# Kernel optimization log

Hardware: AMD Instinct MI355X
Metric: run time of the kernel (lower is better)

The kernel has to match this reference:

```python
import jax, jax.numpy as jnp
import numpy as np

B, S, E, H = 2, 2048, 2048, 32
D = E // H  # head_dim = 64
SCALE = D ** -0.5


def setup_inputs() -> dict:
    key = jax.random.key(0)
    ks = jax.random.split(key, 9)
    std = E ** -0.5
    return {
        "hidden_states": jax.random.normal(ks[0], (B, S, E), dtype=jnp.float32),
        "Wq": jax.random.normal(ks[1], (E, E), dtype=jnp.float32) * std,
        "bq": jax.random.normal(ks[2], (E,), dtype=jnp.float32) * 0.02,
        "Wk": jax.random.normal(ks[3], (E, E), dtype=jnp.float32) * std,
        "bk": jax.random.normal(ks[4], (E,), dtype=jnp.float32) * 0.02,
        "Wv": jax.random.normal(ks[5], (E, E), dtype=jnp.float32) * std,
        "bv": jax.random.normal(ks[6], (E,), dtype=jnp.float32) * 0.02,
        "Wo": jax.random.normal(ks[7], (E, E), dtype=jnp.float32) * std,
        "bo": jax.random.normal(ks[8], (E,), dtype=jnp.float32) * 0.02,
    }


def reference(hidden_states, Wq, bq, Wk, bk, Wv, bv, Wo, bo):
    # QKV projections (torch Linear: x @ W.T + b)
    q = hidden_states @ Wq.T + bq  # [B,S,E]
    k = hidden_states @ Wk.T + bk
    v = hidden_states @ Wv.T + bv
    # split heads -> [B,S,H,D]
    q = q.reshape(B, S, H, D)
    k = k.reshape(B, S, H, D)
    v = v.reshape(B, S, H, D)
    # causal scaled dot-product attention (prefill path of paged attention)
    scores = jnp.einsum("bqhd,bkhd->bhqk", q, k) * SCALE  # [B,H,S,S]
    causal = jnp.tril(jnp.ones((S, S), dtype=bool))
    scores = jnp.where(causal, scores, jnp.finfo(scores.dtype).min)
    probs = jax.nn.softmax(scores, axis=-1)
    attn = jnp.einsum("bhqk,bkhd->bqhd", probs, v).reshape(B, S, E)
    # output projection
    return attn @ Wo.T + bo
```

## Files before the change

kernel.cpp:

```cpp
#include <hip/hip_runtime.h>
#include <hip/hip_bf16.h>

#define B_ 2
#define S_ 2048
#define E_ 2048
#define H_ 32
#define D_ 64
#define SCALE_L2E 0.18033688f

typedef __attribute__((ext_vector_type(8))) short short8_t;
typedef __attribute__((ext_vector_type(4))) float float4_t;
typedef __attribute__((ext_vector_type(16))) float f32x16;
typedef unsigned int uint;
typedef __attribute__((ext_vector_type(4))) uint uint4_t;

__device__ __forceinline__ short f2bf(float f) {
  union { float f; unsigned u; } x; x.f = f;
  unsigned r = x.u + 0x7fffu + ((x.u >> 16) & 1u);
  return (short)(r >> 16);
}

__device__ __forceinline__ void gload_lds16(const void* g, void* l) {
  __builtin_amdgcn_global_load_lds((const __attribute__((address_space(1))) void*)g,
                                   (__attribute__((address_space(3))) void*)l, 16, 0, 0);
}

__device__ __forceinline__ uint cvt_pk_bf16(float lo, float hi) {
  uint r;
  asm volatile("v_cvt_pk_bf16_f32 %0, %1, %2" : "=v"(r) : "v"(lo), "v"(hi));
  return r;
}

__device__ __forceinline__ void pl32swap(uint& a, uint& b) {
  asm volatile("v_permlane32_swap_b32 %0, %1" : "+v"(a), "+v"(b));
}

__device__ __forceinline__ f32x16 zero16() {
  f32x16 v;
#pragma unroll
  for (int i = 0; i < 16; ++i) v[i] = 0.f;
  return v;
}

__global__ void cast_xw(const float* __restrict__ X, const float* __restrict__ Wq,
                        const float* __restrict__ Wk, const float* __restrict__ Wv,
                        short* __restrict__ out) {
  constexpr int nX = 1 << 21, nW = 1 << 20, total = nX + 3 * nW;
  const int stride = gridDim.x * blockDim.x;
  for (int j = blockIdx.x * blockDim.x + threadIdx.x; j < total; j += stride) {
    const float* src;
    int idx;
    if (j < nX) {
      src = X; idx = j;
    } else {
      const int jw = j - nX;
      const int sel = jw >> 20;
      idx = jw & (nW - 1);
      src = sel == 0 ? Wq : (sel == 1 ? Wk : Wv);
    }
    const float4 v = ((const float4*)src)[idx];
    short4 r;
    r.x = f2bf(v.x); r.y = f2bf(v.y); r.z = f2bf(v.z); r.w = f2bf(v.w);
    ((short4*)out)[j] = r;
  }
}

__global__ void cast_bf16_kernel(const float* __restrict__ in, short* __restrict__ out, int n4) {
  const int stride = gridDim.x * blockDim.x;
  for (int j = blockIdx.x * blockDim.x + threadIdx.x; j < n4; j += stride) {
    const float4 v = ((const float4*)in)[j];
    short4 r;
    r.x = f2bf(v.x); r.y = f2bf(v.y); r.z = f2bf(v.z); r.w = f2bf(v.w);
    ((short4*)out)[j] = r;
  }
}

__global__ __launch_bounds__(512, 2) void gemm256_qk(const short* __restrict__ A,
                                                     const short* __restrict__ Wt,
                                                     const float* __restrict__ bq,
                                                     const float* __restrict__ bk,
                                                     short* __restrict__ Qb,
                                                     short* __restrict__ Kb) {
  extern __shared__ __align__(16) char lds[];
  constexpr int K = E_, NT = K / 64;
  const int tid = threadIdx.x, w = tid >> 6, lane = tid & 63;
  const int wr = w >> 2, wc = w & 3;
  const int m0 = blockIdx.y * 256, n0 = blockIdx.x * 256;
  const int l15 = lane & 15, l4 = lane >> 4;

  const int sr = lane >> 2;
  const int ss = lane & 3;
  const char* aB[2];
  const char* bB[2];
#pragma unroll
  for (int g = 0; g < 2; ++g) {
    const int r = w * 32 + g * 16 + sr;
    aB[g] = (const char*)A + (size_t)(m0 + r) * (K * 2) + ((ss ^ ((r >> 1) & 3)) * 16);
    bB[g] = (const char*)Wt + (size_t)(n0 + r) * (K * 2) + ((ss ^ ((r >> 1) & 3)) * 16);
  }

  auto stageA = [&](int buf, int ks, int kt) {
#pragma unroll
    for (int g = 0; g < 2; ++g)
      gload_lds16(aB[g] + kt * 128 + ks * 64, lds + (buf * 2 + ks) * 16384 + w * 2048 + g * 1024);
  };
  auto stageB = [&](int buf, int ks, int kt) {
#pragma unroll
    for (int g = 0; g < 2; ++g)
      gload_lds16(bB[g] + kt * 128 + ks * 64,
                  lds + 65536 + (buf * 2 + ks) * 16384 + w * 2048 + g * 1024);
  };
  auto ldA = [&](int buf, int ks, int i) {
    const int lr = wr * 128 + i * 16 + l15;
    return *(const short8_t*)(lds + (buf * 2 + ks) * 16384 + lr * 64 +
                              ((l4 * 16) ^ (((lr >> 1) & 3) << 4)));
  };
  auto ldB = [&](int buf, int ks, int j) {
    const int lc = wc * 64 + j * 16 + l15;
    return *(const short8_t*)(lds + 65536 + (buf * 2 + ks) * 16384 + lc * 64 +
                              ((l4 * 16) ^ (((lc >> 1) & 3) << 4)));
  };

  float4_t acc[8][4];
#pragma unroll
  for (int i = 0; i < 8; ++i)
#pragma unroll
    for (int j = 0; j < 4; ++j) acc[i][j] = (float4_t){0.f, 0.f, 0.f, 0.f};

  stageA(0, 0, 0);
  stageB(0, 0, 0);
  stageA(0, 1, 0);
  stageB(0, 1, 0);

  short8_t a_[8], b_[4];
  for (int t = 0; t < NT; ++t) {
    const int c = t & 1;
#pragma unroll
    for (int ks = 0; ks < 2; ++ks) {
      if (t + 1 < NT) {
        stageA(c ^ 1, ks, t + 1);
        stageB(c ^ 1, ks, t + 1);
        asm volatile("s_waitcnt vmcnt(8)" ::: "memory");
      } else if (ks == 0) {
        asm volatile("s_waitcnt vmcnt(4)" ::: "memory");
      } else {
        asm volatile("s_waitcnt vmcnt(0)" ::: "memory");
      }
      __builtin_amdgcn_s_barrier();
      asm volatile("" ::: "memory");
#pragma unroll
      for (int i = 0; i < 8; ++i) a_[i] = ldA(c, ks, i);
#pragma unroll
      for (int j = 0; j < 4; ++j) b_[j] = ldB(c, ks, j);
      asm volatile("s_waitcnt lgkmcnt(0)" ::: "memory");
      __builtin_amdgcn_sched_barrier(0);
      __builtin_amdgcn_s_setprio(1);
#pragma unroll
      for (int i = 0; i < 8; ++i)
#pragma unroll
        for (int j = 0; j < 4; ++j)
          acc[i][j] = __builtin_amdgcn_mfma_f32_16x16x32_bf16(a_[i], b_[j], acc[i][j], 0, 0, 0);
      __builtin_amdgcn_s_setprio(0);
    }
  }

  const int seg = n0 >> 11;
  const int ncol = n0 & 2047;
  const float* bias = seg ? bk : bq;
  short* Out = seg ? Kb : Qb;
  const float sc = seg ? 1.0f : SCALE_L2E;
  const int rg = l4 * 4;
#pragma unroll
  for (int j = 0; j < 4; ++j) {
    const int col = ncol + wc * 64 + j * 16 + l15;
    const float bvv = bias[col];
#pragma unroll
    for (int i = 0; i < 8; ++i)
#pragma unroll
      for (int ii = 0; ii < 4; ++ii)
        Out[(size_t)(m0 + wr * 128 + i * 16 + rg + ii) * E_ + col] =
            f2bf((acc[i][j][ii] + bvv) * sc);
  }
}

__global__ __launch_bounds__(512, 2) void gemm_v128(const short* __restrict__ A,
                                                    const short* __restrict__ Wt,
                                                    const float* __restrict__ bv,
                                                    short* __restrict__ Vb) {
  extern __shared__ __align__(16) char lds[];
  constexpr int K = E_, NT = K / 64;
  const int tid = threadIdx.x, w = tid >> 6, lane = tid & 63;
  const int wr = w >> 2, wc = w & 3;
  const int m0 = blockIdx.y * 128, n0 = blockIdx.x * 256;
  const int l15 = lane & 15, l4 = lane >> 4;

  const int sr = lane >> 2;
  const int ss = lane & 3;
  const char* aBase;
  const char* bBase0;
  const char* bBase1;
  {
    const int ra = w * 16 + sr;
    aBase = (const char*)A + (size_t)(m0 + ra) * (K * 2) + ((ss ^ ((ra >> 1) & 3)) * 16);
    const int rb0 = w * 16 + sr;
    bBase0 = (const char*)Wt + (size_t)(n0 + rb0) * (K * 2) + ((ss ^ ((rb0 >> 1) & 3)) * 16);
    const int rb1 = 128 + w * 16 + sr;
    bBase1 = (const char*)Wt + (size_t)(n0 + rb1) * (K * 2) + ((ss ^ ((rb1 >> 1) & 3)) * 16);
  }

  auto stageA = [&](int dbuf, int ks, int kt) {
    gload_lds16(aBase + kt * 128 + ks * 64, lds + (dbuf * 2 + ks) * 8192 + w * 1024);
  };
  auto stageB = [&](int dbuf, int ks, int kt) {
    char* base = lds + 32768 + (dbuf * 2 + ks) * 16384 + w * 1024;
    gload_lds16(bBase0 + kt * 128 + ks * 64, base);
    gload_lds16(bBase1 + kt * 128 + ks * 64, base + 8192);
  };
  auto ldA = [&](int dbuf, int ks, int i) {
    const int lr = wr * 64 + i * 16 + l15;
    return *(const short8_t*)(lds + (dbuf * 2 + ks) * 8192 + lr * 64 +
                              ((l4 * 16) ^ (((lr >> 1) & 3) << 4)));
  };
  auto ldB = [&](int dbuf, int ks, int j) {
    const int lc = wc * 64 + j * 16 + l15;
    return *(const short8_t*)(lds + 32768 + (dbuf * 2 + ks) * 16384 + lc * 64 +
                              ((l4 * 16) ^ (((lc >> 1) & 3) << 4)));
  };

  float4_t acc[4][4];
#pragma unroll
  for (int i = 0; i < 4; ++i)
#pragma unroll
    for (int j = 0; j < 4; ++j) acc[i][j] = (float4_t){0.f, 0.f, 0.f, 0.f};

  stageA(0, 0, 0);
  stageB(0, 0, 0);
  stageA(0, 1, 0);
  stageB(0, 1, 0);

  short8_t a_[4], b_[4];
  for (int t = 0; t < NT; ++t) {
    const int c = t & 1;
#pragma unroll
    for (int ks = 0; ks < 2; ++ks) {
      if (t + 1 < NT) {
        stageA(c ^ 1, ks, t + 1);
        stageB(c ^ 1, ks, t + 1);
        asm volatile("s_waitcnt vmcnt(6)" ::: "memory");
      } else if (ks == 0) {
        asm volatile("s_waitcnt vmcnt(3)" ::: "memory");
      } else {
        asm volatile("s_waitcnt vmcnt(0)" ::: "memory");
      }
      __builtin_amdgcn_s_barrier();
      asm volatile("" ::: "memory");
#pragma unroll
      for (int i = 0; i < 4; ++i) a_[i] = ldA(c, ks, i);
#pragma unroll
      for (int j = 0; j < 4; ++j) b_[j] = ldB(c, ks, j);
      asm volatile("s_waitcnt lgkmcnt(0)" ::: "memory");
      __builtin_amdgcn_sched_barrier(0);
      __builtin_amdgcn_s_setprio(1);
#pragma unroll
      for (int i = 0; i < 4; ++i)
#pragma unroll
        for (int j = 0; j < 4; ++j)
          acc[i][j] = __builtin_amdgcn_mfma_f32_16x16x32_bf16(a_[i], b_[j], acc[i][j], 0, 0, 0);
      __builtin_amdgcn_s_setprio(0);
    }
  }

  __syncthreads();
  const int rg = l4 * 4;
  const int b = m0 >> 11;
  const int mloc = m0 & (S_ - 1);
  char* scratch = lds + w * 2048;
#pragma unroll
  for (int j = 0; j < 4; ++j) {
    const int ncol = n0 + wc * 64 + j * 16;
    const float bvv = bv[ncol + l15];
    asm volatile("" ::: "memory");
#pragma unroll
    for (int i = 0; i < 4; ++i) {
      short4 v;
      v.x = f2bf(acc[i][j][0] + bvv);
      v.y = f2bf(acc[i][j][1] + bvv);
      v.z = f2bf(acc[i][j][2] + bvv);
      v.w = f2bf(acc[i][j][3] + bvv);
      *(short4*)(scratch + l15 * 128 + (((i * 16 + rg) * 2) ^ ((l15 & 7) << 4))) = v;
    }
    asm volatile("s_waitcnt lgkmcnt(0)" ::: "memory");
    __builtin_amdgcn_sched_barrier(0);
#pragma unroll
    for (int half = 0; half < 2; ++half) {
      const int n = (lane >> 3) + half * 8;
      const int mb = (lane & 7) * 16;
      const short8_t vv = *(const short8_t*)(scratch + n * 128 + (mb ^ ((n & 7) << 4)));
      *(short8_t*)(Vb + ((size_t)(b * E_ + ncol + n)) * S_ + mloc + wr * 64 + (mb >> 1)) = vv;
    }
    asm volatile("s_waitcnt lgkmcnt(0)" ::: "memory");
    __builtin_amdgcn_sched_barrier(0);
  }
}

__global__ __launch_bounds__(512, 2) void gemm_o8(const short* __restrict__ A,
                                                  const short* __restrict__ Wt,
                                                  const float* __restrict__ bias,
                                                  float* __restrict__ Fout) {
  extern __shared__ __align__(16) char lds[];
  constexpr int K = E_, NT = K / 64;
  const int tid = threadIdx.x, w = tid >> 6, lane = tid & 63;
  const int wr = w >> 2, wc = w & 3;
  const int m0 = blockIdx.y * 128, n0 = blockIdx.x * 256;
  const int l15 = lane & 15, l4 = lane >> 4;

  const int sr = lane >> 2;
  const int ss = lane & 3;
  const char* aBase;
  const char* bBase0;
  const char* bBase1;
  {
    const int ra = w * 16 + sr;
    aBase = (const char*)A + (size_t)(m0 + ra) * (K * 2) + ((ss ^ ((ra >> 1) & 3)) * 16);
    const int rb0 = w * 16 + sr;
    bBase0 = (const char*)Wt + (size_t)(n0 + rb0) * (K * 2) + ((ss ^ ((rb0 >> 1) & 3)) * 16);
    const int rb1 = 128 + w * 16 + sr;
    bBase1 = (const char*)Wt + (size_t)(n0 + rb1) * (K * 2) + ((ss ^ ((rb1 >> 1) & 3)) * 16);
  }

  auto stageA = [&](int dbuf, int ks, int kt) {
    gload_lds16(aBase + kt * 128 + ks * 64, lds + (dbuf * 2 + ks) * 8192 + w * 1024);
  };
  auto stageB = [&](int dbuf, int ks, int kt) {
    char* base = lds + 32768 + (dbuf * 2 + ks) * 16384 + w * 1024;
    gload_lds16(bBase0 + kt * 128 + ks * 64, base);
    gload_lds16(bBase1 + kt * 128 + ks * 64, base + 8192);
  };
  auto ldA = [&](int dbuf, int ks, int i) {
    const int lr = wr * 64 + i * 16 + l15;
    return *(const short8_t*)(lds + (dbuf * 2 + ks) * 8192 + lr * 64 +
                              ((l4 * 16) ^ (((lr >> 1) & 3) << 4)));
  };
  auto ldB = [&](int dbuf, int ks, int j) {
    const int lc = wc * 64 + j * 16 + l15;
    return *(const short8_t*)(lds + 32768 + (dbuf * 2 + ks) * 16384 + lc * 64 +
                              ((l4 * 16) ^ (((lc >> 1) & 3) << 4)));
  };

  float4_t acc[4][4];
#pragma unroll
  for (int i = 0; i < 4; ++i)
#pragma unroll
    for (int j = 0; j < 4; ++j) acc[i][j] = (float4_t){0.f, 0.f, 0.f, 0.f};

  stageA(0, 0, 0);
  stageB(0, 0, 0);
  stageA(0, 1, 0);
  stageB(0, 1, 0);

  short8_t a_[4], b_[4];
  for (int t = 0; t < NT; ++t) {
    const int c = t & 1;
#pragma unroll
    for (int ks = 0; ks < 2; ++ks) {
      if (t + 1 < NT) {
        stageA(c ^ 1, ks, t + 1);
        stageB(c ^ 1, ks, t + 1);
        asm volatile("s_waitcnt vmcnt(6)" ::: "memory");
      } else if (ks == 0) {
        asm volatile("s_waitcnt vmcnt(3)" ::: "memory");
      } else {
        asm volatile("s_waitcnt vmcnt(0)" ::: "memory");
      }
      __builtin_amdgcn_s_barrier();
      asm volatile("" ::: "memory");
#pragma unroll
      for (int i = 0; i < 4; ++i) a_[i] = ldA(c, ks, i);
#pragma unroll
      for (int j = 0; j < 4; ++j) b_[j] = ldB(c, ks, j);
      asm volatile("s_waitcnt lgkmcnt(0)" ::: "memory");
      __builtin_amdgcn_sched_barrier(0);
      __builtin_amdgcn_s_setprio(1);
#pragma unroll
      for (int i = 0; i < 4; ++i)
#pragma unroll
        for (int j = 0; j < 4; ++j)
          acc[i][j] = __builtin_amdgcn_mfma_f32_16x16x32_bf16(a_[i], b_[j], acc[i][j], 0, 0, 0);
      __builtin_amdgcn_s_setprio(0);
    }
  }

  const int rg = l4 * 4;
#pragma unroll
  for (int j = 0; j < 4; ++j) {
    const int col = n0 + wc * 64 + j * 16 + l15;
    const float bvv = bias[col];
#pragma unroll
    for (int i = 0; i < 4; ++i)
#pragma unroll
      for (int ii = 0; ii < 4; ++ii)
        Fout[(size_t)(m0 + wr * 64 + i * 16 + rg + ii) * E_ + col] = acc[i][j][ii] + bvv;
  }
}

__global__ __launch_bounds__(512, 2) void attn_fwd(const short* __restrict__ Qg,
                                                   const short* __restrict__ Kg,
                                                   const short* __restrict__ Vt,
                                                   short* __restrict__ Og) {
  __shared__ __align__(16) short lds[16384];
  const int tid = threadIdx.x, w = tid >> 6, lane = tid & 63;
  const int l31 = lane & 31, hh = lane >> 5;
  const int bh = blockIdx.x;
  const int b = bh >> 5, h = bh & 31;
  const int pq = blockIdx.y;

  const char* Kgb = (const char*)(Kg + (size_t)b * S_ * E_ + h * D_);
  const char* Vgb = (const char*)(Vt + (size_t)bh * 64 * S_);

  const int srow = w * 8 + (lane >> 3);
  const int sb = (lane & 7) * 16;
  const int ssw = (srow & 7) << 4;

#pragma unroll 1
  for (int ph = 0; ph < 2; ++ph) {
    const int qt = ph ? (7 - pq) : pq;
    const int q0 = qt * 256;
    const int qwmin = q0 + w * 32;
    const int qg = qwmin + l31;

    const short* qr = Qg + ((size_t)(b * S_ + qg)) * E_ + h * D_;
    short8_t qf[4];
#pragma unroll
    for (int dblk = 0; dblk < 4; ++dblk)
      qf[dblk] = *(const short8_t*)(qr + dblk * 16 + hh * 8);

    f32x16 o0 = zero16(), o1 = zero16();
    float m_run = -1e30f, l_run = 0.f;

    const int nt = 4 * qt + 4;
    const int ntw = (qwmin + 31) / 64 + 1;

    gload_lds16(Kgb + (size_t)srow * 4096 + (sb ^ ssw), lds + w * 512);
    gload_lds16(Vgb + (size_t)srow * 4096 + (sb ^ ssw), lds + 4096 + w * 512);
    __syncthreads();

    int cur = 0;
    for (int t = 0; t < nt; ++t) {
      if (t + 1 < nt) {
        const int k0n = (t + 1) * 64;
        short* kb = lds + (cur ^ 1) * 8192 + w * 512;
        gload_lds16(Kgb + (size_t)(k0n + srow) * 4096 + (sb ^ ssw), kb);
        gload_lds16(Vgb + (size_t)srow * 4096 + (size_t)k0n * 2 + (sb ^ ssw), kb + 4096);
      }

      if (t < ntw) {
        const int k0 = t * 64;
        const char* Kc = (const char*)lds + cur * 16384;
        const char* Vc = Kc + 8192;
        const int xs = (l31 & 7) << 4;

        f32x16 st0 = zero16(), st1 = zero16();
#pragma unroll
        for (int dblk = 0; dblk < 4; ++dblk) {
          const int off = (dblk * 32 + hh * 16) ^ xs;
          const short8_t kf0 = *(const short8_t*)(Kc + l31 * 128 + off);
          const short8_t kf1 = *(const short8_t*)(Kc + (32 + l31) * 128 + off);
          st0 = __builtin_amdgcn_mfma_f32_32x32x16_bf16(kf0, qf[dblk], st0, 0, 0, 0);
          st1 = __builtin_amdgcn_mfma_f32_32x32x16_bf16(kf1, qf[dblk], st1, 0, 0, 0);
        }

        if (k0 + 63 > qwmin) {
#pragma unroll
          for (int r = 0; r < 16; ++r) {
            const int kvr = k0 + ((r & 3) + 8 * (r >> 2) + 4 * hh);
            if (kvr > qg) st0[r] = -1e30f;
            if (kvr + 32 > qg) st1[r] = -1e30f;
          }
        }

        float mv = -1e30f;
#pragma unroll
        for (int r = 0; r < 16; ++r) mv = fmaxf(mv, fmaxf(st0[r], st1[r]));
        mv = fmaxf(mv, __shfl_xor(mv, 32));
        const float mnew = fmaxf(m_run, mv);
        const float alpha = exp2f(m_run - mnew);
        m_run = mnew;
        float sum = 0.f;
#pragma unroll
        for (int r = 0; r < 16; ++r) {
          st0[r] = exp2f(st0[r] - mnew);
          st1[r] = exp2f(st1[r] - mnew);
          sum += st0[r] + st1[r];
        }
        sum += __shfl_xor(sum, 32);
        l_run = l_run * alpha + sum;
        o0 = o0 * alpha;
        o1 = o1 * alpha;

        uint pk_[16];
#pragma unroll
        for (int j = 0; j < 8; ++j) pk_[j] = cvt_pk_bf16(st0[2 * j], st0[2 * j + 1]);
#pragma unroll
        for (int j = 0; j < 8; ++j) pk_[8 + j] = cvt_pk_bf16(st1[2 * j], st1[2 * j + 1]);
        pl32swap(pk_[0], pk_[2]);  pl32swap(pk_[1], pk_[3]);
        pl32swap(pk_[4], pk_[6]);  pl32swap(pk_[5], pk_[7]);
        pl32swap(pk_[8], pk_[10]); pl32swap(pk_[9], pk_[11]);
        pl32swap(pk_[12], pk_[14]); pl32swap(pk_[13], pk_[15]);
        uint4_t paw[4];
#pragma unroll
        for (int f = 0; f < 4; ++f)
          paw[f] = (uint4_t){pk_[4 * f], pk_[4 * f + 1], pk_[4 * f + 2], pk_[4 * f + 3]};

#pragma unroll
        for (int kb = 0; kb < 4; ++kb) {
          const short8_t pa = *(const short8_t*)&paw[kb];
          const int off = (kb * 32 + hh * 16) ^ xs;
          const short8_t vf0 = *(const short8_t*)(Vc + l31 * 128 + off);
          const short8_t vf1 = *(const short8_t*)(Vc + (32 + l31) * 128 + off);
          o0 = __builtin_amdgcn_mfma_f32_32x32x16_bf16(vf0, pa, o0, 0, 0, 0);
          o1 = __builtin_amdgcn_mfma_f32_32x32x16_bf16(vf1, pa, o1, 0, 0, 0);
        }
      }

      __syncthreads();
      cur ^= 1;
    }

    {
      short* ow = lds + w * 2048;
      const float inv = 1.0f / l_run;
#pragma unroll
      for (int r = 0; r < 16; ++r) {
        const int d = (r & 3) + 8 * (r >> 2) + 4 * hh;
        const int x = (l31 & 7) << 4;
        *(short*)((char*)ow + l31 * 128 + ((d * 2) ^ x)) = f2bf(o0[r] * inv);
        *(short*)((char*)ow + l31 * 128 + (((d + 32) * 2) ^ x)) = f2bf(o1[r] * inv);
      }
#pragma unroll
      for (int pz = 0; pz < 4; ++pz) {
        const int qloc = pz * 8 + (lane >> 3);
        const int sbyte = (lane & 7) * 16;
        const short8_t vv = *(const short8_t*)((char*)ow + qloc * 128 + (sbyte ^ ((qloc & 7) << 4)));
        *(short8_t*)(Og + ((size_t)(b * S_ + q0 + w * 32 + qloc)) * E_ + h * 64 + (lane & 7) * 8) = vv;
      }
    }
    __syncthreads();
  }
}

extern "C" void kernel_launch(void* const* d_in, const int* in_sizes, int n_in,
                              void* d_out, int out_size, void* d_ws, size_t ws_size,
                              hipStream_t stream) {
  const float* X  = (const float*)d_in[0];
  const float* Wq = (const float*)d_in[1];
  const float* bq = (const float*)d_in[2];
  const float* Wk = (const float*)d_in[3];
  const float* bk = (const float*)d_in[4];
  const float* Wv = (const float*)d_in[5];
  const float* bv = (const float*)d_in[6];
  const float* Wo = (const float*)d_in[7];
  const float* bo = (const float*)d_in[8];

  const size_t NX = (size_t)B_ * S_ * E_;
  const size_t NW = (size_t)E_ * E_;

  short* ws = (short*)d_ws;
  short* Xb = ws;
  short* Wb = Xb + NX;
  short* Kb = Wb + 3 * NW;
  short* Vb = Kb + NX;
  short* Qb = (short*)d_out;
  short* Ab = Xb;

  (void)hipFuncSetAttribute((const void*)gemm256_qk,
                            hipFuncAttributeMaxDynamicSharedMemorySize, 131072);
  (void)hipFuncSetAttribute((const void*)gemm_v128,
                            hipFuncAttributeMaxDynamicSharedMemorySize, 98304);
  (void)hipFuncSetAttribute((const void*)gemm_o8,
                            hipFuncAttributeMaxDynamicSharedMemorySize, 98304);

  cast_xw<<<2048, 256, 0, stream>>>(X, Wq, Wk, Wv, Xb);

  gemm256_qk<<<dim3(16, 16), 512, 131072, stream>>>(Xb, Wb, bq, bk, Qb, Kb);
  gemm_v128<<<dim3(8, 32), 512, 98304, stream>>>(Xb, Wb + 2 * NW, bv, Vb);

  cast_bf16_kernel<<<1024, 256, 0, stream>>>(Wo, Wb, (int)(NW / 4));

  attn_fwd<<<dim3(B_ * H_, 4), 512, 0, stream>>>(Qb, Kb, Vb, Ab);

  gemm_o8<<<dim3(E_ / 256, B_ * S_ / 128), 512, 98304, stream>>>(Ab, Wb, bo, (float*)d_out);
}
```

Measured before the change: 258.9 us.

## Add lazy softmax rescale, tree reductions, and MFMA priority hints in attention

Result: no change. 257.2 us (-0.7%).

```diff
diff --git a/kernel.cpp b/kernel.cpp
--- a/kernel.cpp
+++ b/kernel.cpp
@@ -460,6 +460,7 @@
         const int xs = (l31 & 7) << 4;
 
         f32x16 st0 = zero16(), st1 = zero16();
+        __builtin_amdgcn_s_setprio(1);
 #pragma unroll
         for (int dblk = 0; dblk < 4; ++dblk) {
           const int off = (dblk * 32 + hh * 16) ^ xs;
@@ -468,6 +469,7 @@
           st0 = __builtin_amdgcn_mfma_f32_32x32x16_bf16(kf0, qf[dblk], st0, 0, 0, 0);
           st1 = __builtin_amdgcn_mfma_f32_32x32x16_bf16(kf1, qf[dblk], st1, 0, 0, 0);
         }
+        __builtin_amdgcn_s_setprio(0);
 
         if (k0 + 63 > qwmin) {
 #pragma unroll
@@ -478,24 +480,38 @@
           }
         }
 
-        float mv = -1e30f;
-#pragma unroll
-        for (int r = 0; r < 16; ++r) mv = fmaxf(mv, fmaxf(st0[r], st1[r]));
-        mv = fmaxf(mv, __shfl_xor(mv, 32));
-        const float mnew = fmaxf(m_run, mv);
-        const float alpha = exp2f(m_run - mnew);
-        m_run = mnew;
-        float sum = 0.f;
+        float mx[8];
+#pragma unroll
+        for (int r = 0; r < 8; ++r)
+          mx[r] = fmaxf(fmaxf(st0[r], st0[r + 8]), fmaxf(st1[r], st1[r + 8]));
+#pragma unroll
+        for (int s = 4; s > 0; s >>= 1)
+#pragma unroll
+          for (int i = 0; i < s; ++i) mx[i] = fmaxf(mx[i], mx[i + s]);
+        const float mv = fmaxf(mx[0], __shfl_xor(mx[0], 32));
+
+        if (!__all(mv <= m_run + 8.0f)) {
+          const float mnew = fmaxf(m_run, mv);
+          const float alpha = exp2f(m_run - mnew);
+          m_run = mnew;
+          l_run *= alpha;
+          o0 = o0 * alpha;
+          o1 = o1 * alpha;
+        }
+
 #pragma unroll
         for (int r = 0; r < 16; ++r) {
-          st0[r] = exp2f(st0[r] - mnew);
-          st1[r] = exp2f(st1[r] - mnew);
-          sum += st0[r] + st1[r];
+          st0[r] = exp2f(st0[r] - m_run);
+          st1[r] = exp2f(st1[r] - m_run);
         }
-        sum += __shfl_xor(sum, 32);
-        l_run = l_run * alpha + sum;
-        o0 = o0 * alpha;
-        o1 = o1 * alpha;
+        float sm[8];
+#pragma unroll
+        for (int r = 0; r < 8; ++r) sm[r] = (st0[r] + st0[r + 8]) + (st1[r] + st1[r + 8]);
+#pragma unroll
+        for (int s = 4; s > 0; s >>= 1)
+#pragma unroll
+          for (int i = 0; i < s; ++i) sm[i] += sm[i + s];
+        l_run += sm[0] + __shfl_xor(sm[0], 32);
 
         uint pk_[16];
 #pragma unroll
@@ -511,6 +527,7 @@
         for (int f = 0; f < 4; ++f)
           paw[f] = (uint4_t){pk_[4 * f], pk_[4 * f + 1], pk_[4 * f + 2], pk_[4 * f + 3]};
 
+        __builtin_amdgcn_s_setprio(1);
 #pragma unroll
         for (int kb = 0; kb < 4; ++kb) {
           const short8_t pa = *(const short8_t*)&paw[kb];
@@ -520,6 +537,7 @@
           o0 = __builtin_amdgcn_mfma_f32_32x32x16_bf16(vf0, pa, o0, 0, 0, 0);
           o1 = __builtin_amdgcn_mfma_f32_32x32x16_bf16(vf1, pa, o1, 0, 0, 0);
         }
+        __builtin_amdgcn_s_setprio(0);
       }
 
       __syncthreads();
```
